# Kernel tuning notes

Hardware: AMD Instinct MI355X
Metric: run time of the kernel (lower is better)

## Reference

```python
import jax, jax.numpy as jnp
import numpy as np

B, L = 1024, 1024
LP, STRIDE, WIN = 64, 32, 8   # patch_length, patch_stride, window_size
GH, RH, NC = 64, 128, 11      # gnn hidden, rnn hidden, num_classes


def setup_inputs() -> dict:
    key = jax.random.key(0)
    ks = jax.random.split(key, 16)
    def n(k, shape, s=0.1):
        return jax.random.normal(k, shape, dtype=jnp.float32) * s
    z = lambda *s: jnp.zeros(s, jnp.float32)
    return {
        "I": jax.random.normal(ks[0], (B, L), dtype=jnp.float32),
        "Q": jax.random.normal(ks[1], (B, L), dtype=jnp.float32),
        "edge_weights": jax.random.normal(ks[2], (LP, LP), dtype=jnp.float32),
        "Wn1": n(ks[3], (GH, 2)),  "bn1": z(GH),
        "Ws1": n(ks[4], (GH, 2)),  "bs1": z(GH),
        "Wn2": n(ks[5], (GH, GH)), "bn2": z(GH),
        "Ws2": n(ks[6], (GH, GH)), "bs2": z(GH),
        "Wih0": n(ks[7], (4 * RH, GH)), "Whh0": n(ks[8], (4 * RH, RH)),
        "bih0": z(4 * RH), "bhh0": z(4 * RH),
        "Wih1": n(ks[9], (4 * RH, RH)), "Whh1": n(ks[10], (4 * RH, RH)),
        "bih1": z(4 * RH), "bhh1": z(4 * RH),
        "Wc1": n(ks[11], (64, RH)), "bc1": z(64),
        "Wc2": n(ks[12], (NC, 64)), "bc2": z(NC),
    }


def _sage(x, adj, deg_inv, Wn, bn, Ws, bs):
    # x: [B,P,Lp,d]; adj: [Lp,Lp]; mean-aggregate neighbors then self+neigh linear + relu
    neigh = jnp.einsum('ij,bpjd->bpid', adj, x) * deg_inv
    return jax.nn.relu(jnp.einsum('bpid,od->bpio', x, Ws) + bs
                       + jnp.einsum('bpid,od->bpio', neigh, Wn) + bn)


def _lstm(x, Wih, Whh, bih, bhh):
    # x: [B,T,D]; PyTorch gate order i,f,g,o
    Hd = Whh.shape[1]
    xg = jnp.einsum('btd,gd->btg', x, Wih) + bih + bhh  # [B,T,4H]
    h0 = jnp.zeros((x.shape[0], Hd), x.dtype)
    def step(carry, xt):
        h, c = carry
        g = xt + h @ Whh.T
        i, f, gg, o = jnp.split(g, 4, axis=-1)
        c = jax.nn.sigmoid(f) * c + jax.nn.sigmoid(i) * jnp.tanh(gg)
        h = jax.nn.sigmoid(o) * jnp.tanh(c)
        return (h, c), h
    (h, _), hs = jax.lax.scan(step, (h0, h0), jnp.swapaxes(xg, 0, 1))
    return jnp.swapaxes(hs, 0, 1), h


def _forward(I, Q, edge_weights, Wn1, bn1, Ws1, bs1, Wn2, bn2, Ws2, bs2,
             Wih0, Whh0, bih0, bhh0, Wih1, Whh1, bih1, bhh1, Wc1, bc1, Wc2, bc2):
    Lp = edge_weights.shape[0]
    P = (I.shape[-1] - Lp) // STRIDE + 1
    # vectorized patch extraction: [B,P,Lp,2]
    idx = jnp.arange(P)[:, None] * STRIDE + jnp.arange(Lp)[None, :]
    patches = jnp.stack([I[:, idx], Q[:, idx]], axis=-1)
    # banded adjacency shared across all patches
    r = jnp.arange(Lp)
    mask = ((jnp.abs(r[:, None] - r[None, :]) <= WIN) & (r[:, None] != r[None, :])).astype(jnp.float32)
    adj = jax.nn.sigmoid(edge_weights) * mask
    deg = adj.sum(axis=1, keepdims=True)           # [Lp,1]
    deg_inv = jnp.where(deg > 0, 1.0 / deg, 0.0)
    x = _sage(patches, adj, deg_inv, Wn1, bn1, Ws1, bs1)   # [B,P,Lp,GH]
    x = _sage(x, adj, deg_inv, Wn2, bn2, Ws2, bs2)
    feats = x.sum(axis=2)                                  # [B,P,GH]
    out0, _ = _lstm(feats, Wih0, Whh0, bih0, bhh0)
    _, h = _lstm(out0, Wih1, Whh1, bih1, bhh1)             # last layer final hidden [B,RH]
    hid = jax.nn.relu(h @ Wc1.T + bc1)
    return hid @ Wc2.T + bc2                               # [B,NC]


def reference(I, Q, edge_weights, Wn1, bn1, Ws1, bs1, Wn2, bn2, Ws2, bs2,
              Wih0, Whh0, bih0, bhh0, Wih1, Whh1, bih1, bhh1, Wc1, bc1, Wc2, bc2):
    return _forward(I, Q, edge_weights, Wn1, bn1, Ws1, bs1, Wn2, bn2, Ws2, bs2,
                    Wih0, Whh0, bih0, bhh0, Wih1, Whh1, bih1, bhh1, Wc1, bc1, Wc2, bc2)
```

## Files before the change

### kernel.cpp

```cpp
#include <hip/hip_runtime.h>
#include <hip/hip_bf16.h>
#include <math.h>

#define L_SZ 1024
#define STRIDE_ 32
#define WIN 8
#define PNUM 31
#define NPATCH 31744
#define SGRID 512

#define X1TS 72
#define CAS  136

typedef __attribute__((ext_vector_type(8))) short short8;
typedef __attribute__((ext_vector_type(4))) short short4v;
typedef __attribute__((ext_vector_type(4))) float f32x4;

#define MFMA16(a, b, c) __builtin_amdgcn_mfma_f32_16x16x32_bf16(a, b, c, 0, 0, 0)

__device__ __forceinline__ void bar_lds() {
    __builtin_amdgcn_sched_barrier(0);
    asm volatile("s_waitcnt lgkmcnt(0)" ::: "memory");
    __builtin_amdgcn_s_barrier();
    __builtin_amdgcn_sched_barrier(0);
}

__device__ __forceinline__ float sigf(float x) { return 1.0f / (1.0f + __expf(-x)); }
__device__ __forceinline__ float tanhfast(float x) {
    float ax = fabsf(x);
    float t = __expf(-2.0f * ax);
    return copysignf((1.0f - t) / (1.0f + t), x);
}
__device__ __forceinline__ short f2bf(float f) {
    __hip_bfloat16 h = __float2bfloat16(f);
    return *reinterpret_cast<short*>(&h);
}
__device__ __forceinline__ float bf2f(short s) {
    __hip_bfloat16 h = *reinterpret_cast<__hip_bfloat16*>(&s);
    return __bfloat162float(h);
}

__global__ void adj_kernel(const float* __restrict__ ew, float* __restrict__ adjn) {
    int i = threadIdx.x;
    if (i >= 64) return;
    float sum = 0.f;
    for (int j = 0; j < 64; ++j) {
        int d = i - j; d = d < 0 ? -d : d;
        float a = (d <= WIN && d != 0) ? sigf(ew[i * 64 + j]) : 0.f;
        sum += a;
    }
    float dinv = (sum > 0.f) ? 1.0f / sum : 0.f;
    for (int j = 0; j < 64; ++j) {
        int d = i - j; d = d < 0 ? -d : d;
        float a = (d <= WIN && d != 0) ? sigf(ew[i * 64 + j]) : 0.f;
        adjn[i * 64 + j] = a * dinv;
    }
}

__global__ void prep_kernel(const float* __restrict__ Wih0, const float* __restrict__ Whh0,
                            const float* __restrict__ Wih1, const float* __restrict__ Whh1,
                            const float* __restrict__ adjn,
                            const float* __restrict__ Ws2, const float* __restrict__ Wn2,
                            short* __restrict__ wihf0G, short* __restrict__ wihf1G,
                            short* __restrict__ adjfG, short* __restrict__ wcatfG,
                            short* __restrict__ whhf0G, short* __restrict__ whhf1G) {
    int bid = blockIdx.x, tid = threadIdx.x;
    if (bid < 32) {
        int t = bid * 256 + tid;
        int f = t >> 6, l = t & 63;
        int hl = f & 1, ks = (f >> 1) & 1, nt = f >> 2;
        int q = l >> 4, l15 = l & 15;
        short8 v;
        #pragma unroll
        for (int e = 0; e < 8; ++e) {
            float src = Wih0[(size_t)(nt * 16 + l15) * 64 + ks * 32 + 8 * q + e];
            short hi = f2bf(src);
            v[e] = hl ? f2bf(src - bf2f(hi)) : hi;
        }
        *(short8*)(wihf0G + (size_t)f * 512 + l * 8) = v;
        return;
    }
    if (bid < 96) {
        int t = (bid - 32) * 256 + tid;
        int f = t >> 6, l = t & 63;
        int hl = f & 1, ks = (f >> 1) & 3, nt = f >> 3;
        int q = l >> 4, l15 = l & 15;
        short8 v;
        #pragma unroll
        for (int e = 0; e < 8; ++e) {
            float src = Wih1[(size_t)(nt * 16 + l15) * 128 + ks * 32 + 8 * q + e];
            short hi = f2bf(src);
            v[e] = hl ? f2bf(src - bf2f(hi)) : hi;
        }
        *(short8*)(wihf1G + (size_t)f * 512 + l * 8) = v;
        return;
    }
    if (bid < 106) {
        int t = (bid - 96) * 256 + tid;
        if (t >= 2432) return;
        int f = t >> 6, l = t & 63;
        int q = l >> 4, l15 = l & 15;
        short8 v;
        if (f < 6) {
            const int ntT[6] = {0, 1, 1, 2, 2, 3};
            const int ksT[6] = {0, 0, 1, 0, 1, 1};
            int row = l15 + 16 * ntT[f], col = 8 * q + 32 * ksT[f];
            #pragma unroll
            for (int e = 0; e < 8; ++e)
                v[e] = f2bf(adjn[row * 64 + col + e]);
            *(short8*)(adjfG + ((size_t)f * 64 + l) * 8) = v;
        } else {
            int fi = f - 6;
            int isLo = fi >= 16;
            int ff = isLo ? fi - 16 : fi;
            int nt = ff >> 2, ks = ff & 3;
            int oo = l15 + 16 * nt;
            #pragma unroll
            for (int e = 0; e < 8; ++e) {
                int k = 32 * ks + 8 * q + e;
                float src = (k < 64) ? Ws2[oo * 64 + k] : Wn2[oo * 64 + (k - 64)];
                short hi = f2bf(src);
                v[e] = isLo ? f2bf(src - bf2f(hi)) : hi;
            }
            *(short8*)(wcatfG + ((size_t)fi * 64 + l) * 8) = v;
        }
        return;
    }
    {
        int layer = (bid < 170) ? 0 : 1;
        int base = layer ? 170 : 106;
        const float* Whh = layer ? Whh1 : Whh0;
        short* dst = layer ? whhf1G : whhf0G;
        int t = (bid - base) * 256 + tid;
        int frag = t >> 6, l = t & 63;
        int hl = frag & 1, ks = (frag >> 1) & 3, NT = frag >> 3;
        int g = NT * 16 + (l & 15);
        int kbase = ks * 32 + (l >> 4) * 8;
        short8 v;
        #pragma unroll
        for (int e = 0; e < 8; ++e) {
            float src = Whh[(size_t)g * 128 + kbase + e];
            short hi = f2bf(src);
            v[e] = hl ? f2bf(src - bf2f(hi)) : hi;
        }
        *(short8*)(dst + (size_t)t * 8) = v;
    }
}

__launch_bounds__(256, 2)
__global__ void sage_mfma(const float* __restrict__ I, const float* __restrict__ Q,
                          const float* __restrict__ adjn,
                          const float* __restrict__ Wn1, const float* __restrict__ bn1,
                          const float* __restrict__ Ws1, const float* __restrict__ bs1,
                          const float* __restrict__ bn2, const float* __restrict__ bs2,
                          const short* __restrict__ adjfG, const short* __restrict__ wcatfG,
                          float* __restrict__ feats) {
    __shared__ __align__(16) short s_x1T[2][64 * X1TS];
    __shared__ __align__(16) short s_cat[2][64 * CAS];

    const int tid = threadIdx.x;
    const int w = tid >> 6, l = tid & 63, q = l >> 4, l15 = l & 15;

    const bool hasKs0 = (w <= 2);
    const bool hasKs1 = (w >= 1);
    const int idx0 = (w == 0) ? 0 : (w == 1 ? 1 : 3);
    const int idx1 = (w == 1) ? 2 : (w == 2 ? 4 : 5);
    short8 adjB0 = {}, adjB1 = {};
    if (hasKs0) adjB0 = *(const short8*)(adjfG + ((size_t)idx0 * 64 + l) * 8);
    if (hasKs1) adjB1 = *(const short8*)(adjfG + ((size_t)idx1 * 64 + l) * 8);

    short8 whf[4], wlf[4];
    #pragma unroll
    for (int ks = 0; ks < 4; ++ks) {
        whf[ks] = *(const short8*)(wcatfG + ((size_t)(w * 4 + ks) * 64 + l) * 8);
        wlf[ks] = *(const short8*)(wcatfG + ((size_t)(w * 4 + ks + 16) * 64 + l) * 8);
    }
    const int oo = l15 + 16 * w;
    const float bo = bs2[oo] + bn2[oo];

    float areg[17];
    #pragma unroll
    for (int d = 0; d < 17; ++d) {
        int j = l + d - WIN;
        areg[d] = (j >= 0 && j < 64) ? adjn[l * 64 + j] : 0.f;
    }

    float x0a[2], x0b[2];
    #pragma unroll
    for (int P = 0; P < 2; ++P) {
        int m = blockIdx.x + P * 512;
        int b = m / PNUM, p = m % PNUM;
        x0a[P] = I[(size_t)b * L_SZ + p * STRIDE_ + l];
        x0b[P] = Q[(size_t)b * L_SZ + p * STRIDE_ + l];
    }

    for (int it = 0; it < 31; ++it) {
        const int m0 = it * 1024 + blockIdx.x;

        #pragma unroll
        for (int P = 0; P < 2; ++P) {
            float n0a = 0.f, n0b = 0.f;
            #pragma unroll
            for (int d = 0; d < 17; ++d) {
                int j = l + d - WIN;
                float xa = __shfl(x0a[P], j, 64);
                float xb = __shfl(x0b[P], j, 64);
                n0a += areg[d] * xa;
                n0b += areg[d] * xb;
            }
            union { short s[16]; short8 v[2]; } pk;
            #pragma unroll
            for (int t = 0; t < 16; ++t) {
                int o = w * 16 + t;
                float2 wsv = ((const float2*)Ws1)[o];
                float2 wnv = ((const float2*)Wn1)[o];
                float v = bs1[o] + bn1[o] + wsv.x * x0a[P] + wsv.y * x0b[P]
                                          + wnv.x * n0a + wnv.y * n0b;
                v = fmaxf(v, 0.f);
                short bv = f2bf(v);
                s_x1T[P][o * X1TS + l] = bv;
                pk.s[t] = bv;
            }
            *(short8*)&s_cat[P][l * CAS + w * 16]     = pk.v[0];
            *(short8*)&s_cat[P][l * CAS + w * 16 + 8] = pk.v[1];
        }

        if (it + 1 < 31) {
            #pragma unroll
            for (int P = 0; P < 2; ++P) {
                int m = (it + 1) * 1024 + blockIdx.x + P * 512;
                int b = m / PNUM, p = m % PNUM;
                x0a[P] = I[(size_t)b * L_SZ + p * STRIDE_ + l];
                x0b[P] = Q[(size_t)b * L_SZ + p * STRIDE_ + l];
            }
        }
        bar_lds();

        #pragma unroll
        for (int P = 0; P < 2; ++P) {
            #pragma unroll
            for (int ot = 0; ot < 4; ++ot) {
                f32x4 c = {0.f, 0.f, 0.f, 0.f};
                if (hasKs0) {
                    short8 a = *(const short8*)&s_x1T[P][(16 * ot + l15) * X1TS + 8 * q];
                    c = MFMA16(a, adjB0, c);
                }
                if (hasKs1) {
                    short8 a = *(const short8*)&s_x1T[P][(16 * ot + l15) * X1TS + 8 * q + 32];
                    c = MFMA16(a, adjB1, c);
                }
                short4v nv;
                nv[0] = f2bf(c[0]); nv[1] = f2bf(c[1]);
                nv[2] = f2bf(c[2]); nv[3] = f2bf(c[3]);
                *(short4v*)&s_cat[P][(16 * w + l15) * CAS + 64 + 16 * ot + 4 * q] = nv;
            }
        }
        bar_lds();

        #pragma unroll
        for (int P = 0; P < 2; ++P) {
            f32x4 z = {0.f, 0.f, 0.f, 0.f};
            f32x4 acc2[4] = {z, z, z, z};
            #pragma unroll
            for (int it2 = 0; it2 < 4; ++it2) {
                short8 a2[4];
                #pragma unroll
                for (int ks = 0; ks < 4; ++ks)
                    a2[ks] = *(const short8*)&s_cat[P][(16 * it2 + l15) * CAS + 32 * ks + 8 * q];
                #pragma unroll
                for (int ks = 0; ks < 4; ++ks) {
                    acc2[it2] = MFMA16(a2[ks], whf[ks], acc2[it2]);
                    acc2[it2] = MFMA16(a2[ks], wlf[ks], acc2[it2]);
                }
            }
            float total = 0.f;
            #pragma unroll
            for (int it2 = 0; it2 < 4; ++it2) {
                float s = fmaxf(acc2[it2][0] + bo, 0.f) + fmaxf(acc2[it2][1] + bo, 0.f)
                        + fmaxf(acc2[it2][2] + bo, 0.f) + fmaxf(acc2[it2][3] + bo, 0.f);
                s += __shfl_xor(s, 16);
                s += __shfl_xor(s, 32);
                total += s;
            }
            if (l < 16)
                feats[(size_t)(m0 + P * 512) * 64 + 16 * w + l15] = total;
        }
        bar_lds();
    }
}

template <int K>
__launch_bounds__(256, 2)
__global__ void gemm_mfma(const float* __restrict__ A, const short* __restrict__ wihfG,
                          const float* __restrict__ bias1, const float* __restrict__ bias2,
                          float* __restrict__ C) {
    constexpr int K32 = K / 32;
    constexpr int K4 = K / 4;
    constexpr int AS = (K == 64) ? 72 : 136;
    __shared__ __align__(16) short s_ah[64 * AS];
    __shared__ __align__(16) short s_al[64 * AS];
    const int tid = threadIdx.x;
    const int w = tid >> 6, l = tid & 63, q = l >> 4, l15 = l & 15;
    const int m0 = blockIdx.x * 64;
    const int j0 = blockIdx.y * 128;

    {
        const float4* Ag = (const float4*)(A + (size_t)m0 * K);
        for (int e = tid; e < 16 * K; e += 256) {
            int row = e / K4, c4 = e % K4;
            float4 v = Ag[row * K4 + c4];
            short4v h, lo;
            h[0] = f2bf(v.x); lo[0] = f2bf(v.x - bf2f(h[0]));
            h[1] = f2bf(v.y); lo[1] = f2bf(v.y - bf2f(h[1]));
            h[2] = f2bf(v.z); lo[2] = f2bf(v.z - bf2f(h[2]));
            h[3] = f2bf(v.w); lo[3] = f2bf(v.w - bf2f(h[3]));
            *(short4v*)&s_ah[row * AS + c4 * 4] = h;
            *(short4v*)&s_al[row * AS + c4 * 4] = lo;
        }
    }

    short8 bh[2][K32], bl[2][K32];
    #pragma unroll
    for (int c = 0; c < 2; ++c) {
        int nt = (j0 >> 4) + 2 * w + c;
        #pragma unroll
        for (int ks = 0; ks < K32; ++ks) {
            bh[c][ks] = *(const short8*)(wihfG + (((size_t)(nt * K32 + ks) * 2 + 0) * 64 + l) * 8);
            bl[c][ks] = *(const short8*)(wihfG + (((size_t)(nt * K32 + ks) * 2 + 1) * 64 + l) * 8);
        }
    }
    __syncthreads();

    f32x4 z = {0.f, 0.f, 0.f, 0.f};
    #pragma unroll
    for (int mt = 0; mt < 4; ++mt) {
        f32x4 acc[2] = {z, z};
        #pragma unroll
        for (int ks = 0; ks < K32; ++ks) {
            short8 ah = *(const short8*)&s_ah[(16 * mt + l15) * AS + 32 * ks + 8 * q];
            short8 al = *(const short8*)&s_al[(16 * mt + l15) * AS + 32 * ks + 8 * q];
            #pragma unroll
            for (int c = 0; c < 2; ++c) {
                acc[c] = MFMA16(ah, bh[c][ks], acc[c]);
                acc[c] = MFMA16(al, bh[c][ks], acc[c]);
                acc[c] = MFMA16(ah, bl[c][ks], acc[c]);
            }
        }
        #pragma unroll
        for (int c = 0; c < 2; ++c) {
            int col = j0 + (2 * w + c) * 16 + l15;
            float bo = bias1[col] + bias2[col];
            #pragma unroll
            for (int reg = 0; reg < 4; ++reg) {
                int row = m0 + 16 * mt + 4 * q + reg;
                C[(size_t)row * 512 + col] = acc[c][reg] + bo;
            }
        }
    }
}

#define HS 136
#define GS 516

template <bool FINAL>
__launch_bounds__(512)
__global__ void lstm_mfma(const float* __restrict__ xg, const short* __restrict__ whhfG,
                          float* __restrict__ out0,
                          const float* __restrict__ Wc1, const float* __restrict__ bc1,
                          const float* __restrict__ Wc2, const float* __restrict__ bc2,
                          float* __restrict__ out) {
    __shared__ __align__(16) short s_h[16 * HS];
    __shared__ __align__(16) float s_g2[16 * GS];
    __shared__ __align__(16) float s_hid[4 * 68];
    const int tid = threadIdx.x;
    const int w = tid >> 6, l = tid & 63, quad = l >> 4, l15 = l & 15;
    const int b0 = blockIdx.x * 4;
    const int u = tid & 127, r0 = tid >> 7;

    short8 whf[16], wlf[16];
    #pragma unroll
    for (int nt = 0; nt < 4; ++nt)
        #pragma unroll
        for (int ks = 0; ks < 4; ++ks) {
            size_t NT = (size_t)(w * 4 + nt);
            whf[nt * 4 + ks] = *(const short8*)(whhfG + (((NT * 4 + ks) * 2 + 0) * 64 + l) * 8);
            wlf[nt * 4 + ks] = *(const short8*)(whhfG + (((NT * 4 + ks) * 2 + 1) * 64 + l) * 8);
        }

    float c0 = 0.f;
    for (int e = tid; e < 16 * HS; e += 512) s_h[e] = 0;
    __syncthreads();

    float xgv[4];
    {
        size_t base = ((size_t)(b0 + r0) * PNUM + 0) * 512 + u;
        xgv[0] = xg[base];
        xgv[1] = xg[base + 128];
        xgv[2] = xg[base + 256];
        xgv[3] = xg[base + 384];
    }

    for (int t = 0; t < 31; ++t) {
        short8 af[4];
        #pragma unroll
        for (int ks = 0; ks < 4; ++ks)
            af[ks] = *(const short8*)&s_h[l15 * HS + ks * 32 + quad * 8];
        f32x4 z = {0.f, 0.f, 0.f, 0.f};
        f32x4 acc[4] = {z, z, z, z};
        #pragma unroll
        for (int nt = 0; nt < 4; ++nt)
            #pragma unroll
            for (int ks = 0; ks < 4; ++ks) {
                acc[nt] = MFMA16(af[ks], whf[nt * 4 + ks], acc[nt]);
                acc[nt] = MFMA16(af[ks], wlf[nt * 4 + ks], acc[nt]);
            }
        #pragma unroll
        for (int nt = 0; nt < 4; ++nt) {
            int n = w * 64 + nt * 16 + l15;
            #pragma unroll
            for (int reg = 0; reg < 4; ++reg)
                s_g2[(quad * 4 + reg) * GS + n] = acc[nt][reg];
        }

        float nx0 = 0.f, nx1 = 0.f, nx2 = 0.f, nx3 = 0.f;
        if (t + 1 < 31) {
            size_t base = ((size_t)(b0 + r0) * PNUM + (t + 1)) * 512 + u;
            nx0 = xg[base];
            nx1 = xg[base + 128];
            nx2 = xg[base + 256];
            nx3 = xg[base + 384];
        }
        bar_lds();

        {
            float gi = xgv[0] + s_g2[r0 * GS + u];
            float gf = xgv[1] + s_g2[r0 * GS + 128 + u];
            float gg = xgv[2] + s_g2[r0 * GS + 256 + u];
            float go = xgv[3] + s_g2[r0 * GS + 384 + u];
            float cn = sigf(gf) * c0 + sigf(gi) * tanhfast(gg);
            float h = sigf(go) * tanhfast(cn);
            c0 = cn;
            s_h[r0 * HS + u] = f2bf(h);
            if (!FINAL)
                out0[((size_t)(b0 + r0) * PNUM + t) * 128 + u] = h;
        }
        xgv[0] = nx0; xgv[1] = nx1; xgv[2] = nx2; xgv[3] = nx3;
        bar_lds();
    }

    if (FINAL) {
        if (tid < 256) {
            int rr = tid >> 6, uu = tid & 63;
            float acc = bc1[uu];
            const float* wv = Wc1 + (size_t)uu * 128;
            #pragma unroll 8
            for (int k = 0; k < 128; ++k) acc += wv[k] * bf2f(s_h[rr * HS + k]);
            s_hid[rr * 68 + uu] = fmaxf(acc, 0.f);
        }
        __syncthreads();
        if (tid < 44) {
            int rr = tid / 11, cc = tid % 11;
            float acc = bc2[cc];
            #pragma unroll
            for (int uu = 0; uu < 64; ++uu) acc += Wc2[cc * 64 + uu] * s_hid[rr * 68 + uu];
            out[(size_t)(b0 + rr) * 11 + cc] = acc;
        }
    }
}

extern "C" void kernel_launch(void* const* d_in, const int* in_sizes, int n_in,
                              void* d_out, int out_size, void* d_ws, size_t ws_size,
                              hipStream_t stream) {
    (void)in_sizes; (void)n_in; (void)out_size; (void)ws_size;
    const float* I    = (const float*)d_in[0];
    const float* Q    = (const float*)d_in[1];
    const float* ew   = (const float*)d_in[2];
    const float* Wn1  = (const float*)d_in[3];
    const float* bn1  = (const float*)d_in[4];
    const float* Ws1  = (const float*)d_in[5];
    const float* bs1  = (const float*)d_in[6];
    const float* Wn2  = (const float*)d_in[7];
    const float* bn2  = (const float*)d_in[8];
    const float* Ws2  = (const float*)d_in[9];
    const float* bs2  = (const float*)d_in[10];
    const float* Wih0 = (const float*)d_in[11];
    const float* Whh0 = (const float*)d_in[12];
    const float* bih0 = (const float*)d_in[13];
    const float* bhh0 = (const float*)d_in[14];
    const float* Wih1 = (const float*)d_in[15];
    const float* Whh1 = (const float*)d_in[16];
    const float* bih1 = (const float*)d_in[17];
    const float* bhh1 = (const float*)d_in[18];
    const float* Wc1  = (const float*)d_in[19];
    const float* bc1  = (const float*)d_in[20];
    const float* Wc2  = (const float*)d_in[21];
    const float* bc2  = (const float*)d_in[22];
    float* out = (float*)d_out;

    float* wsp   = (float*)d_ws;
    float* adjn  = wsp;
    short* wihf0G = (short*)(adjn + 4096);
    short* wihf1G = (short*)(adjn + 4096 + 32768);
    short* adjfG  = (short*)(adjn + 4096 + 98304);
    short* wcatfG = adjfG + 3072;
    short* whhf0G = wcatfG + 16384;
    short* whhf1G = whhf0G + 131072;
    float* feats = adjn + 4096 + 98304 + 140800;
    float* out0  = feats + 2031616;
    float* xg    = out0  + 4063232;

    adj_kernel<<<1, 64, 0, stream>>>(ew, adjn);
    prep_kernel<<<234, 256, 0, stream>>>(Wih0, Whh0, Wih1, Whh1, adjn, Ws2, Wn2,
                                         wihf0G, wihf1G, adjfG, wcatfG, whhf0G, whhf1G);
    sage_mfma<<<SGRID, 256, 0, stream>>>(I, Q, adjn, Wn1, bn1, Ws1, bs1,
                                         bn2, bs2, adjfG, wcatfG, feats);
    gemm_mfma<64><<<dim3(496, 4), 256, 0, stream>>>(feats, wihf0G, bih0, bhh0, xg);
    lstm_mfma<false><<<256, 512, 0, stream>>>(xg, whhf0G, out0,
                                              nullptr, nullptr, nullptr, nullptr, nullptr);
    gemm_mfma<128><<<dim3(496, 4), 256, 0, stream>>>(out0, wihf1G, bih1, bhh1, xg);
    lstm_mfma<true><<<256, 512, 0, stream>>>(xg, whhf1G, nullptr,
                                             Wc1, bc1, Wc2, bc2, out);
}
```

Measured before the change: 423.5 us.

## Permute LSTM weight tiles so each lane holds all four gates in registers

The recurrent weight fragments are reassigned so each wave's four N-tiles hold the i,f,g,o gates of the same 16 hidden units. The gate nonlinearity can then be computed directly from MFMA accumulators in registers. This drops the LDS gate buffer and one of the two barriers per timestep. In exchange, only quad 0 lanes (16 of 64 per wave) do the elementwise update and xg loads, so elementwise parallelism drops and register use grows.

```diff
diff --git a/kernel.cpp b/kernel.cpp
--- a/kernel.cpp
+++ b/kernel.cpp
@@ -360,7 +360,6 @@
 }
 
 #define HS 136
-#define GS 516
 
 template <bool FINAL>
 __launch_bounds__(512)
@@ -370,34 +369,36 @@
                           const float* __restrict__ Wc2, const float* __restrict__ bc2,
                           float* __restrict__ out) {
     __shared__ __align__(16) short s_h[16 * HS];
-    __shared__ __align__(16) float s_g2[16 * GS];
     __shared__ __align__(16) float s_hid[4 * 68];
     const int tid = threadIdx.x;
     const int w = tid >> 6, l = tid & 63, quad = l >> 4, l15 = l & 15;
     const int b0 = blockIdx.x * 4;
-    const int u = tid & 127, r0 = tid >> 7;
+    const int j = 16 * w + l15;
 
     short8 whf[16], wlf[16];
     #pragma unroll
     for (int nt = 0; nt < 4; ++nt)
         #pragma unroll
         for (int ks = 0; ks < 4; ++ks) {
-            size_t NT = (size_t)(w * 4 + nt);
+            size_t NT = (size_t)(w + 8 * nt);
             whf[nt * 4 + ks] = *(const short8*)(whhfG + (((NT * 4 + ks) * 2 + 0) * 64 + l) * 8);
             wlf[nt * 4 + ks] = *(const short8*)(whhfG + (((NT * 4 + ks) * 2 + 1) * 64 + l) * 8);
         }
 
-    float c0 = 0.f;
+    float c4[4] = {0.f, 0.f, 0.f, 0.f};
+    float xgv[16];
     for (int e = tid; e < 16 * HS; e += 512) s_h[e] = 0;
     __syncthreads();
 
-    float xgv[4];
-    {
-        size_t base = ((size_t)(b0 + r0) * PNUM + 0) * 512 + u;
-        xgv[0] = xg[base];
-        xgv[1] = xg[base + 128];
-        xgv[2] = xg[base + 256];
-        xgv[3] = xg[base + 384];
+    if (quad == 0) {
+        #pragma unroll
+        for (int r = 0; r < 4; ++r) {
+            size_t base = ((size_t)(b0 + r) * PNUM + 0) * 512 + j;
+            xgv[4 * r + 0] = xg[base];
+            xgv[4 * r + 1] = xg[base + 128];
+            xgv[4 * r + 2] = xg[base + 256];
+            xgv[4 * r + 3] = xg[base + 384];
+        }
     }
 
     for (int t = 0; t < 31; ++t) {
@@ -414,37 +415,36 @@
                 acc[nt] = MFMA16(af[ks], whf[nt * 4 + ks], acc[nt]);
                 acc[nt] = MFMA16(af[ks], wlf[nt * 4 + ks], acc[nt]);
             }
-        #pragma unroll
-        for (int nt = 0; nt < 4; ++nt) {
-            int n = w * 64 + nt * 16 + l15;
-            #pragma unroll
-            for (int reg = 0; reg < 4; ++reg)
-                s_g2[(quad * 4 + reg) * GS + n] = acc[nt][reg];
-        }
-
-        float nx0 = 0.f, nx1 = 0.f, nx2 = 0.f, nx3 = 0.f;
-        if (t + 1 < 31) {
-            size_t base = ((size_t)(b0 + r0) * PNUM + (t + 1)) * 512 + u;
-            nx0 = xg[base];
-            nx1 = xg[base + 128];
-            nx2 = xg[base + 256];
-            nx3 = xg[base + 384];
-        }
-        bar_lds();
-
-        {
-            float gi = xgv[0] + s_g2[r0 * GS + u];
-            float gf = xgv[1] + s_g2[r0 * GS + 128 + u];
-            float gg = xgv[2] + s_g2[r0 * GS + 256 + u];
-            float go = xgv[3] + s_g2[r0 * GS + 384 + u];
-            float cn = sigf(gf) * c0 + sigf(gi) * tanhfast(gg);
-            float h = sigf(go) * tanhfast(cn);
-            c0 = cn;
-            s_h[r0 * HS + u] = f2bf(h);
-            if (!FINAL)
-                out0[((size_t)(b0 + r0) * PNUM + t) * 128 + u] = h;
-        }
-        xgv[0] = nx0; xgv[1] = nx1; xgv[2] = nx2; xgv[3] = nx3;
+
+        float nx[16];
+        if (quad == 0 && t + 1 < 31) {
+            #pragma unroll
+            for (int r = 0; r < 4; ++r) {
+                size_t base = ((size_t)(b0 + r) * PNUM + (t + 1)) * 512 + j;
+                nx[4 * r + 0] = xg[base];
+                nx[4 * r + 1] = xg[base + 128];
+                nx[4 * r + 2] = xg[base + 256];
+                nx[4 * r + 3] = xg[base + 384];
+            }
+        }
+
+        if (quad == 0) {
+            #pragma unroll
+            for (int r = 0; r < 4; ++r) {
+                float gi = xgv[4 * r + 0] + acc[0][r];
+                float gf = xgv[4 * r + 1] + acc[1][r];
+                float gg = xgv[4 * r + 2] + acc[2][r];
+                float go = xgv[4 * r + 3] + acc[3][r];
+                float cn = sigf(gf) * c4[r] + sigf(gi) * tanhfast(gg);
+                float h = sigf(go) * tanhfast(cn);
+                c4[r] = cn;
+                s_h[r * HS + j] = f2bf(h);
+                if (!FINAL)
+                    out0[((size_t)(b0 + r) * PNUM + t) * 128 + j] = h;
+            }
+            #pragma unroll
+            for (int e = 0; e < 16; ++e) xgv[e] = nx[e];
+        }
         bar_lds();
     }
 
```

New measurement: 459.5 us. 8.5% more time.

## Keep LSTM gate tiles in registers via lane shuffles instead of LDS staging

Applied to the files above, without the earlier changes.

Reassigns each wave's MFMA output tiles so that all four gates (i,f,g,o) of a hidden unit land in the same lane group, by interleaving N-tiles with stride 8 across waves. The gates are then pulled to the owning lanes with cross-lane shuffles instead of being written to and read back from a shared gate buffer. This removes the s_g2 LDS round trip and its LDS traffic each timestep, and moves one barrier to right after the h reads. In exchange it adds shuffle and select instructions, and it relies on the rows padded past the 4 real batch rows being discarded.

```diff
diff --git a/kernel.cpp b/kernel.cpp
--- a/kernel.cpp
+++ b/kernel.cpp
@@ -360,7 +360,6 @@
 }
 
 #define HS 136
-#define GS 516
 
 template <bool FINAL>
 __launch_bounds__(512)
@@ -370,19 +369,19 @@
                           const float* __restrict__ Wc2, const float* __restrict__ bc2,
                           float* __restrict__ out) {
     __shared__ __align__(16) short s_h[16 * HS];
-    __shared__ __align__(16) float s_g2[16 * GS];
     __shared__ __align__(16) float s_hid[4 * 68];
     const int tid = threadIdx.x;
     const int w = tid >> 6, l = tid & 63, quad = l >> 4, l15 = l & 15;
     const int b0 = blockIdx.x * 4;
-    const int u = tid & 127, r0 = tid >> 7;
+    const int j = 16 * w + l15;
+    const int row = quad;
 
     short8 whf[16], wlf[16];
     #pragma unroll
     for (int nt = 0; nt < 4; ++nt)
         #pragma unroll
         for (int ks = 0; ks < 4; ++ks) {
-            size_t NT = (size_t)(w * 4 + nt);
+            size_t NT = (size_t)(w + 8 * nt);
             whf[nt * 4 + ks] = *(const short8*)(whhfG + (((NT * 4 + ks) * 2 + 0) * 64 + l) * 8);
             wlf[nt * 4 + ks] = *(const short8*)(whhfG + (((NT * 4 + ks) * 2 + 1) * 64 + l) * 8);
         }
@@ -393,7 +392,7 @@
 
     float xgv[4];
     {
-        size_t base = ((size_t)(b0 + r0) * PNUM + 0) * 512 + u;
+        size_t base = ((size_t)(b0 + row) * PNUM + 0) * 512 + j;
         xgv[0] = xg[base];
         xgv[1] = xg[base + 128];
         xgv[2] = xg[base + 256];
@@ -405,6 +404,8 @@
         #pragma unroll
         for (int ks = 0; ks < 4; ++ks)
             af[ks] = *(const short8*)&s_h[l15 * HS + ks * 32 + quad * 8];
+        bar_lds();
+
         f32x4 z = {0.f, 0.f, 0.f, 0.f};
         f32x4 acc[4] = {z, z, z, z};
         #pragma unroll
@@ -414,35 +415,37 @@
                 acc[nt] = MFMA16(af[ks], whf[nt * 4 + ks], acc[nt]);
                 acc[nt] = MFMA16(af[ks], wlf[nt * 4 + ks], acc[nt]);
             }
-        #pragma unroll
-        for (int nt = 0; nt < 4; ++nt) {
-            int n = w * 64 + nt * 16 + l15;
-            #pragma unroll
-            for (int reg = 0; reg < 4; ++reg)
-                s_g2[(quad * 4 + reg) * GS + n] = acc[nt][reg];
-        }
 
         float nx0 = 0.f, nx1 = 0.f, nx2 = 0.f, nx3 = 0.f;
         if (t + 1 < 31) {
-            size_t base = ((size_t)(b0 + r0) * PNUM + (t + 1)) * 512 + u;
+            size_t base = ((size_t)(b0 + row) * PNUM + (t + 1)) * 512 + j;
             nx0 = xg[base];
             nx1 = xg[base + 128];
             nx2 = xg[base + 256];
             nx3 = xg[base + 384];
         }
-        bar_lds();
+
+        float g4[4];
+        #pragma unroll
+        for (int nt = 0; nt < 4; ++nt) {
+            float s0 = __shfl(acc[nt][0], l15, 64);
+            float s1 = __shfl(acc[nt][1], l15, 64);
+            float s2 = __shfl(acc[nt][2], l15, 64);
+            float s3 = __shfl(acc[nt][3], l15, 64);
+            g4[nt] = (quad == 0) ? s0 : (quad == 1) ? s1 : (quad == 2) ? s2 : s3;
+        }
 
         {
-            float gi = xgv[0] + s_g2[r0 * GS + u];
-            float gf = xgv[1] + s_g2[r0 * GS + 128 + u];
-            float gg = xgv[2] + s_g2[r0 * GS + 256 + u];
-            float go = xgv[3] + s_g2[r0 * GS + 384 + u];
+            float gi = xgv[0] + g4[0];
+            float gf = xgv[1] + g4[1];
+            float gg = xgv[2] + g4[2];
+            float go = xgv[3] + g4[3];
             float cn = sigf(gf) * c0 + sigf(gi) * tanhfast(gg);
             float h = sigf(go) * tanhfast(cn);
             c0 = cn;
-            s_h[r0 * HS + u] = f2bf(h);
+            s_h[row * HS + j] = f2bf(h);
             if (!FINAL)
-                out0[((size_t)(b0 + r0) * PNUM + t) * 128 + u] = h;
+                out0[((size_t)(b0 + row) * PNUM + t) * 128 + j] = h;
         }
         xgv[0] = nx0; xgv[1] = nx1; xgv[2] = nx2; xgv[3] = nx3;
         bar_lds();
```

Measured after the change: 406.3 us, median of 2. 4.1% less time.
